# Performance work log

Hardware: AMD Instinct MI355X
Metric: run time of the kernel (lower is better)

Reference implementation:

```python
import jax, jax.numpy as jnp
import numpy as np

B, N, DIM = 16, 1024, 768


def setup_inputs() -> dict:
    key = jax.random.key(0)
    ks = jax.random.split(key, 8)
    x = jax.random.normal(ks[0], (B, N, DIM), dtype=jnp.float32)
    y = jax.random.normal(ks[1], (B, N, DIM), dtype=jnp.float32)
    coords = jax.random.normal(ks[2], (N, N, 6), dtype=jnp.float32)
    # orthogonal init for U (as in torch init.orthogonal_)
    a = jax.random.normal(ks[3], (DIM, DIM), dtype=jnp.float32)
    q, r = jnp.linalg.qr(a)
    U = q * jnp.sign(jnp.diagonal(r))[None, :]
    S1 = jnp.ones((DIM,), dtype=jnp.float32)
    S2 = jnp.ones((DIM,), dtype=jnp.float32)
    gating = jnp.asarray(1.0, dtype=jnp.float32)
    temp = jnp.asarray(0.1, dtype=jnp.float32)
    pos_emb = jnp.zeros((N, 6, 1), dtype=jnp.float32)
    return {"x": x, "y": y, "coords": coords, "U": U, "S1": S1, "S2": S2,
            "gating": gating, "temp": temp, "pos_emb": pos_emb}


def reference(x, y, coords, U, S1, S2, gating, temp, pos_emb):
    dim = x.shape[-1]
    scale = dim ** (-0.5)
    # spectral decomposition: x @ U^T @ diag(S^2) @ U
    xu = x @ U.T                                   # [B,N,d]
    x1 = (xu * jnp.square(S1)) @ U                 # [B,N,d]
    x2 = (xu * jnp.square(S2)) @ U                 # [B,N,d]
    xs = jnp.stack([x1, x2], axis=1)               # [B,2,N,d]
    patch_score = jax.nn.softmax(
        jnp.einsum('bknd,bmd->bknm', xs, y) * scale, axis=-1)  # [B,2,N,M]
    pos = jnp.squeeze(coords @ pos_emb, -1)        # [N,M]
    pos_score = jax.nn.softmax(pos, axis=-1)[None, None]        # [1,1,N,M]
    g = jax.nn.sigmoid(gating)
    attn = (1.0 - g) * patch_score + g * pos_score  # [B,2,N,M]
    # entropy-routed gating
    entropy = jnp.sum(-attn * jnp.log(attn + 1e-8), axis=-1)    # [B,2,N]
    hmap = 2.0 - 2.0 * jax.nn.sigmoid(temp * jnp.transpose(entropy, (0, 2, 1)))  # [B,N,2]
    fgbg = hmap[..., 0] >= hmap[..., 1]
    route = jax.lax.stop_gradient(
        jnp.stack([fgbg, ~fgbg], axis=-1).astype(hmap.dtype))   # [B,N,2]
    heat_map = jnp.sum(hmap * route, axis=-1, keepdims=True)    # [B,N,1]
    attn_c = jnp.sum(attn * jnp.transpose(route, (0, 2, 1))[..., None], axis=1)  # [B,N,M]
    out = attn_c @ y                               # [B,N,d]
    return (out, heat_map)
```

## Files before the change

### kernel.cpp

```cpp
#include <hip/hip_runtime.h>
#include <hip/hip_bf16.h>

#define DEV __device__ __forceinline__

typedef unsigned short u16;
typedef short short8 __attribute__((ext_vector_type(8)));
typedef float f32x16 __attribute__((ext_vector_type(16)));

static const int BB = 16;
static const int NN = 1024;
static const int DD = 768;

DEV u16 f2bf(float f) {
    unsigned u = __builtin_bit_cast(unsigned, f);
    unsigned r = u + 0x7fffu + ((u >> 16) & 1u);
    return (u16)(r >> 16);
}
DEV float h2f(u16 u) { return (float)__builtin_bit_cast(_Float16, u); }
DEV u16 f2h(float f) { return __builtin_bit_cast(u16, (_Float16)f); }

DEV short8 ldf8_bf(const float* p) {
    float4 f0 = *(const float4*)p;
    float4 f1 = *(const float4*)(p + 4);
    short8 r;
    r[0] = (short)f2bf(f0.x); r[1] = (short)f2bf(f0.y);
    r[2] = (short)f2bf(f0.z); r[3] = (short)f2bf(f0.w);
    r[4] = (short)f2bf(f1.x); r[5] = (short)f2bf(f1.y);
    r[6] = (short)f2bf(f1.z); r[7] = (short)f2bf(f1.w);
    return r;
}

DEV void gl_lds16(const u16* g, u16* l) {
    __builtin_amdgcn_global_load_lds(
        (const __attribute__((address_space(1))) unsigned int*)g,
        (__attribute__((address_space(3))) unsigned int*)l, 16, 0, 0);
}

template<int OM>
__global__ __launch_bounds__(256, 3) void gemm128(
    const u16* __restrict__ Ag, const u16* __restrict__ Bg, void* __restrict__ Cg,
    int K, int N, int zmod,
    long sA0, long sA1, long sB0, long sB1, long sC0, long sC1,
    float scale)
{
    __shared__ u16 As[128 * 64];
    __shared__ u16 Bs[128 * 64];

    int z = blockIdx.z;
    const u16* A = Ag + (long)(z % zmod) * sA0 + (long)(z / zmod) * sA1;
    const u16* B = Bg + (long)(z % zmod) * sB0 + (long)(z / zmod) * sB1;
    u16*   Cu = (u16*)Cg   + (long)(z % zmod) * sC0 + (long)(z / zmod) * sC1;
    float* Cf = (float*)Cg + (long)(z % zmod) * sC0 + (long)(z / zmod) * sC1;

    int tid  = threadIdx.x;
    int lane = tid & 63, wave = tid >> 6;
    int wm = wave & 1, wn = wave >> 1;
    int ln31 = lane & 31, khalf = lane >> 5;

    long m0 = (long)blockIdx.x * 128;
    long n0 = (long)blockIdx.y * 128;

    long aOfs[4], bOfs[4];
    u16 *lA[4], *lB[4];
#pragma unroll
    for (int i = 0; i < 4; i++) {
        int p = tid + i * 256;
        int row = p >> 3, qs = p & 7;
        int q = qs ^ (row & 7);
        aOfs[i] = (m0 + row) * (long)K + q * 8;
        bOfs[i] = (n0 + row) * (long)K + q * 8;
        lA[i] = As + p * 8;
        lB[i] = Bs + p * 8;
    }

    int aoff[2][4], boff[2][4];
#pragma unroll
    for (int t = 0; t < 2; t++) {
        int ra = wm * 64 + t * 32 + ln31;
        int rb = wn * 64 + t * 32 + ln31;
#pragma unroll
        for (int h = 0; h < 4; h++) {
            aoff[t][h] = ra * 64 + (((h * 2 + khalf) ^ (ra & 7)) * 8);
            boff[t][h] = rb * 64 + (((h * 2 + khalf) ^ (rb & 7)) * 8);
        }
    }

    f32x16 acc[2][2] = {};

    for (int k0 = 0; k0 < K; k0 += 64) {
#pragma unroll
        for (int i = 0; i < 4; i++) gl_lds16(A + aOfs[i] + k0, lA[i]);
#pragma unroll
        for (int i = 0; i < 4; i++) gl_lds16(B + bOfs[i] + k0, lB[i]);
        __syncthreads();

#pragma unroll
        for (int h = 0; h < 4; h++) {
            short8 af[2], bfr[2];
#pragma unroll
            for (int t = 0; t < 2; t++) af[t]  = *(const short8*)(As + aoff[t][h]);
#pragma unroll
            for (int t = 0; t < 2; t++) bfr[t] = *(const short8*)(Bs + boff[t][h]);
#pragma unroll
            for (int ti = 0; ti < 2; ti++)
#pragma unroll
                for (int tj = 0; tj < 2; tj++)
                    acc[ti][tj] = __builtin_amdgcn_mfma_f32_32x32x16_bf16(
                        af[ti], bfr[tj], acc[ti][tj], 0, 0, 0);
        }
        __syncthreads();
    }

    long crow = m0 + wm * 64 + 4 * khalf;
    long ccol = n0 + wn * 64 + ln31;
#pragma unroll
    for (int ti = 0; ti < 2; ti++)
#pragma unroll
        for (int tj = 0; tj < 2; tj++)
#pragma unroll
            for (int r = 0; r < 16; r++) {
                long row = crow + ti * 32 + (r & 3) + 8 * (r >> 2);
                long col = ccol + tj * 32;
                float v = acc[ti][tj][r] * scale;
                long idx = row * (long)N + col;
                if constexpr (OM == 0)      Cu[idx] = f2bf(v);
                else if constexpr (OM == 1) Cu[idx] = f2h(v);
                else                        Cf[idx] = v;
            }
}

DEV float wave_red_max(float v) {
#pragma unroll
    for (int o = 32; o; o >>= 1) v = fmaxf(v, __shfl_xor(v, o));
    return v;
}
DEV float wave_red_sum(float v) {
#pragma unroll
    for (int o = 32; o; o >>= 1) v += __shfl_xor(v, o);
    return v;
}
DEV float block_red_max(float v, float* sh) {
    v = wave_red_max(v);
    if ((threadIdx.x & 63) == 0) sh[threadIdx.x >> 6] = v;
    __syncthreads();
    v = fmaxf(fmaxf(sh[0], sh[1]), fmaxf(sh[2], sh[3]));
    __syncthreads();
    return v;
}
DEV float block_red_sum(float v, float* sh) {
    v = wave_red_sum(v);
    if ((threadIdx.x & 63) == 0) sh[threadIdx.x >> 6] = v;
    __syncthreads();
    v = (sh[0] + sh[1]) + (sh[2] + sh[3]);
    __syncthreads();
    return v;
}

__global__ __launch_bounds__(256) void k_prep_all(
    const float* __restrict__ x, const float* __restrict__ y,
    const float* __restrict__ coords, const float* __restrict__ U,
    const float* __restrict__ S1, const float* __restrict__ S2,
    const float* __restrict__ pe,
    u16* __restrict__ xb, u16* __restrict__ yb, u16* __restrict__ yT,
    u16* __restrict__ UTb, u16* __restrict__ VT1, u16* __restrict__ VT2,
    float* __restrict__ P)
{
    __shared__ float shmem[32 * 33];
    int bid = blockIdx.x, tid = threadIdx.x;

    if (bid < 6144) {
        long i = ((long)bid * 256 + tid) * 8;
        *(short8*)(xb + i) = ldf8_bf(x + i);
        return;
    }
    bid -= 6144;

    if (bid < 12288) {
        float (*tile)[33] = (float(*)[33])shmem;
        int b = bid / 768, rem = bid % 768;
        int d0 = (rem % 24) * 32, m0 = (rem / 24) * 32;
        int tx = tid & 31, ty = tid >> 5;
        const float* ybase = y + (long)b * NN * DD;
#pragma unroll
        for (int r = 0; r < 32; r += 8) {
            int m = m0 + ty + r, d = d0 + tx;
            float v = ybase[(long)m * DD + d];
            tile[ty + r][tx] = v;
            yb[(long)b * NN * DD + (long)m * DD + d] = f2bf(v);
        }
        __syncthreads();
#pragma unroll
        for (int r = 0; r < 32; r += 8) {
            int d = d0 + ty + r, m = m0 + tx;
            yT[(long)b * DD * NN + (long)d * NN + m] = f2bf(tile[tx][ty + r]);
        }
        return;
    }
    bid -= 12288;

    if (bid < 1024) {
        int n = bid, t = tid;
        float p6[6];
#pragma unroll
        for (int c = 0; c < 6; c++) p6[c] = pe[n * 6 + c];
        float v[4];
#pragma unroll
        for (int i = 0; i < 4; i++) {
            const float* cp = coords + ((long)n * NN + t * 4 + i) * 6;
            v[i] = p6[0]*cp[0] + p6[1]*cp[1] + p6[2]*cp[2]
                 + p6[3]*cp[3] + p6[4]*cp[4] + p6[5]*cp[5];
        }
        float mx = block_red_max(fmaxf(fmaxf(v[0], v[1]), fmaxf(v[2], v[3])), shmem);
        float e[4], s = 0.f;
#pragma unroll
        for (int i = 0; i < 4; i++) { e[i] = expf(v[i] - mx); s += e[i]; }
        float Z = block_red_sum(s, shmem);
        float inv = 1.f / Z;
        float4 o; o.x = e[0]*inv; o.y = e[1]*inv; o.z = e[2]*inv; o.w = e[3]*inv;
        *(float4*)(P + ((long)n << 10) + t * 4) = o;
        return;
    }
    bid -= 1024;

    {
        float (*tile)[33] = (float(*)[33])shmem;
        int i0 = (bid % 24) * 32, j0 = (bid / 24) * 32;
        int tx = tid & 31, ty = tid >> 5;
#pragma unroll
        for (int r = 0; r < 32; r += 8) {
            int i = i0 + ty + r, j = j0 + tx;
            tile[ty + r][tx] = U[(long)i * DD + j];
        }
        __syncthreads();
        float s1v = S1[i0 + tx];
        float s2v = S2[i0 + tx];
        s1v *= s1v; s2v *= s2v;
#pragma unroll
        for (int r = 0; r < 32; r += 8) {
            int j = j0 + ty + r, i = i0 + tx;
            float v = tile[tx][ty + r];
            UTb[(long)j * DD + i] = f2bf(v);
            VT1[(long)j * DD + i] = f2bf(s1v * v);
            VT2[(long)j * DD + i] = f2bf(s2v * v);
        }
    }
}

__global__ __launch_bounds__(256) void k_route(
    u16* __restrict__ S, const float* __restrict__ P,
    const float* __restrict__ gating, const float* __restrict__ temp,
    float* __restrict__ heat)
{
    __shared__ float sh[4];
    int bn = blockIdx.x;
    int b = bn >> 10, n = bn & 1023, t = threadIdx.x;
    u16* s1p = S + ((long)(b * 2) << 20) + ((long)n << 10) + t * 4;
    u16* s2p = s1p + (1L << 20);
    const float* pp = P + ((long)n << 10) + t * 4;

    ushort4 r1 = *(const ushort4*)s1p;
    ushort4 r2 = *(const ushort4*)s2p;
    float4 pv = *(const float4*)pp;
    float s1[4] = { h2f(r1.x), h2f(r1.y), h2f(r1.z), h2f(r1.w) };
    float s2[4] = { h2f(r2.x), h2f(r2.y), h2f(r2.z), h2f(r2.w) };
    float p4[4] = { pv.x, pv.y, pv.z, pv.w };

    float mx1 = block_red_max(fmaxf(fmaxf(s1[0], s1[1]), fmaxf(s1[2], s1[3])), sh);
    float mx2 = block_red_max(fmaxf(fmaxf(s2[0], s2[1]), fmaxf(s2[2], s2[3])), sh);

    float e1[4], e2[4], z1 = 0.f, z2 = 0.f;
#pragma unroll
    for (int i = 0; i < 4; i++) {
        e1[i] = expf(s1[i] - mx1); z1 += e1[i];
        e2[i] = expf(s2[i] - mx2); z2 += e2[i];
    }
    float Z1 = block_red_sum(z1, sh);
    float Z2 = block_red_sum(z2, sh);

    float g = 1.f / (1.f + expf(-gating[0]));
    float c1 = (1.f - g) / Z1, c2 = (1.f - g) / Z2;

    float a1[4], a2[4], hh1 = 0.f, hh2 = 0.f;
#pragma unroll
    for (int i = 0; i < 4; i++) {
        a1[i] = e1[i] * c1 + g * p4[i];
        a2[i] = e2[i] * c2 + g * p4[i];
        hh1 -= a1[i] * logf(a1[i] + 1e-8f);
        hh2 -= a2[i] * logf(a2[i] + 1e-8f);
    }
    float H1 = block_red_sum(hh1, sh);
    float H2 = block_red_sum(hh2, sh);

    float tv = temp[0];
    float hm0 = 2.f - 2.f / (1.f + expf(-tv * H1));
    float hm1 = 2.f - 2.f / (1.f + expf(-tv * H2));
    int ks = (hm0 >= hm1) ? 0 : 1;
    if (t == 0) heat[bn] = ks ? hm1 : hm0;

    ushort4 w;
    w.x = f2bf(ks ? a2[0] : a1[0]);
    w.y = f2bf(ks ? a2[1] : a1[1]);
    w.z = f2bf(ks ? a2[2] : a1[2]);
    w.w = f2bf(ks ? a2[3] : a1[3]);
    *(ushort4*)s1p = w;
}

extern "C" void kernel_launch(void* const* d_in, const int* in_sizes, int n_in,
                              void* d_out, int out_size, void* d_ws, size_t ws_size,
                              hipStream_t stream)
{
    (void)in_sizes; (void)n_in; (void)out_size; (void)ws_size;
    const float* x      = (const float*)d_in[0];
    const float* y      = (const float*)d_in[1];
    const float* coords = (const float*)d_in[2];
    const float* U      = (const float*)d_in[3];
    const float* S1     = (const float*)d_in[4];
    const float* S2     = (const float*)d_in[5];
    const float* gating = (const float*)d_in[6];
    const float* temp   = (const float*)d_in[7];
    const float* pose   = (const float*)d_in[8];

    float* out  = (float*)d_out;
    float* heat = out + (long)BB * NN * DD;

    char* w = (char*)d_ws;
    u16* UTb = (u16*)w;  w += (long)DD * DD * 2;
    u16* VT  = (u16*)w;  w += (long)2 * DD * DD * 2;
    u16* W2  = (u16*)w;  w += (long)2 * DD * DD * 2;
    u16* xb  = (u16*)w;  w += (long)BB * NN * DD * 2;
    u16* x12 = (u16*)w;  w += (long)2 * BB * NN * DD * 2;
    u16* yb  = (u16*)w;  w += (long)BB * NN * DD * 2;
    u16* yT  = (u16*)w;  w += (long)BB * DD * NN * 2;
    u16* S   = (u16*)w;  w += (long)BB * 2 * NN * NN * 2;
    float* P = (float*)w;

    const long MBN = (long)BB * NN * DD;
    const long BND = (long)NN * DD;
    const long SPL = (long)NN * NN;
    const long DSQ = (long)DD * DD;

    k_prep_all<<<dim3(20032), dim3(256), 0, stream>>>(
        x, y, coords, U, S1, S2, pose, xb, yb, yT, UTb, VT, VT + DSQ, P);

    gemm128<0><<<dim3(DD / 128, DD / 128, 2), dim3(256), 0, stream>>>(
        UTb, VT, W2, DD, DD, 2,
        0L, 0L, DSQ, 0L, DSQ, 0L, 1.0f);

    gemm128<0><<<dim3(BB * NN / 128, DD / 128, 2), dim3(256), 0, stream>>>(
        xb, W2, x12, DD, DD, 2,
        0L, 0L, DSQ, 0L, MBN, 0L, 1.0f);

    gemm128<1><<<dim3(NN / 128, NN / 128, BB * 2), dim3(256), 0, stream>>>(
        x12, yb, S, DD, NN, 2,
        MBN, BND, 0L, BND, SPL, 2 * SPL, 0.036084391824351615f);

    k_route<<<dim3(BB * NN), dim3(256), 0, stream>>>(S, P, gating, temp, heat);

    gemm128<2><<<dim3(NN / 128, DD / 128, BB), dim3(256), 0, stream>>>(
        S, yT, out, NN, DD, 1,
        0L, 2 * SPL, 0L, BND, 0L, BND, 1.0f);
}
```

Measured before the change: 384.6 us.

## Fuse x fp32-to-bf16 conversion into GEMM loads and widen route kernel rows

Removes the separate pass that converts x to bf16. A new GEMM variant loads fp32 A tiles straight into LDS and packs them to bf16 with truncating byte permutes before each MFMA. This avoids writing and rereading a bf16 copy of x, at the cost of twice the LDS and global traffic for A tiles and round-toward-zero rather than round-to-nearest conversion. Separately, the routing kernel now uses 128 threads with 8 elements each, so its block reductions span two waves instead of four.

```diff
diff --git a/kernel.cpp b/kernel.cpp
--- a/kernel.cpp
+++ b/kernel.cpp
@@ -30,10 +30,15 @@
     return r;
 }
 
-DEV void gl_lds16(const u16* g, u16* l) {
+DEV void gl_lds16(const void* g, void* l) {
     __builtin_amdgcn_global_load_lds(
         (const __attribute__((address_space(1))) unsigned int*)g,
         (__attribute__((address_space(3))) unsigned int*)l, 16, 0, 0);
+}
+
+DEV unsigned pkbf_rtz(float f0, float f1) {
+    return __builtin_amdgcn_perm(__builtin_bit_cast(unsigned, f1),
+                                 __builtin_bit_cast(unsigned, f0), 0x07060302u);
 }
 
 template<int OM>
@@ -129,6 +134,105 @@
             }
 }
 
+__global__ __launch_bounds__(256, 3) void gemm_f32a(
+    const float* __restrict__ Ag, const u16* __restrict__ Bg, u16* __restrict__ Cg,
+    int K, int N, long sB0, long sC0)
+{
+    __shared__ float As[128 * 64];
+    __shared__ u16   Bs[128 * 64];
+
+    int z = blockIdx.z;
+    const u16* B = Bg + (long)z * sB0;
+    u16* Cu = Cg + (long)z * sC0;
+
+    int tid  = threadIdx.x;
+    int lane = tid & 63, wave = tid >> 6;
+    int wm = wave & 1, wn = wave >> 1;
+    int ln31 = lane & 31, khalf = lane >> 5;
+
+    long m0 = (long)blockIdx.x * 128;
+    long n0 = (long)blockIdx.y * 128;
+
+    long aOfs[8]; float* lA[8];
+#pragma unroll
+    for (int i = 0; i < 8; i++) {
+        int p = tid + i * 256;
+        int row = p >> 4, q = (p & 15) ^ (row & 15);
+        aOfs[i] = (m0 + row) * (long)K + q * 4;
+        lA[i] = As + p * 4;
+    }
+    long bOfs[4]; u16* lB[4];
+#pragma unroll
+    for (int i = 0; i < 4; i++) {
+        int p = tid + i * 256;
+        int row = p >> 3, q = (p & 7) ^ (row & 7);
+        bOfs[i] = (n0 + row) * (long)K + q * 8;
+        lB[i] = Bs + p * 8;
+    }
+
+    int aoff[2][4][2], boff[2][4];
+#pragma unroll
+    for (int t = 0; t < 2; t++) {
+        int ra = wm * 64 + t * 32 + ln31;
+        int rb = wn * 64 + t * 32 + ln31;
+#pragma unroll
+        for (int h = 0; h < 4; h++) {
+            int c0 = h * 4 + khalf * 2;
+            aoff[t][h][0] = ra * 64 + ((c0 ^ (ra & 15)) * 4);
+            aoff[t][h][1] = ra * 64 + (((c0 + 1) ^ (ra & 15)) * 4);
+            boff[t][h] = rb * 64 + (((h * 2 + khalf) ^ (rb & 7)) * 8);
+        }
+    }
+
+    f32x16 acc[2][2] = {};
+
+    for (int k0 = 0; k0 < K; k0 += 64) {
+#pragma unroll
+        for (int i = 0; i < 8; i++) gl_lds16(Ag + aOfs[i] + k0, lA[i]);
+#pragma unroll
+        for (int i = 0; i < 4; i++) gl_lds16(B + bOfs[i] + k0, lB[i]);
+        __syncthreads();
+
+#pragma unroll
+        for (int h = 0; h < 4; h++) {
+            short8 af[2], bfr[2];
+#pragma unroll
+            for (int t = 0; t < 2; t++) {
+                float4 v0 = *(const float4*)(As + aoff[t][h][0]);
+                float4 v1 = *(const float4*)(As + aoff[t][h][1]);
+                uint4 wv;
+                wv.x = pkbf_rtz(v0.x, v0.y);
+                wv.y = pkbf_rtz(v0.z, v0.w);
+                wv.z = pkbf_rtz(v1.x, v1.y);
+                wv.w = pkbf_rtz(v1.z, v1.w);
+                af[t] = __builtin_bit_cast(short8, wv);
+            }
+#pragma unroll
+            for (int t = 0; t < 2; t++) bfr[t] = *(const short8*)(Bs + boff[t][h]);
+#pragma unroll
+            for (int ti = 0; ti < 2; ti++)
+#pragma unroll
+                for (int tj = 0; tj < 2; tj++)
+                    acc[ti][tj] = __builtin_amdgcn_mfma_f32_32x32x16_bf16(
+                        af[ti], bfr[tj], acc[ti][tj], 0, 0, 0);
+        }
+        __syncthreads();
+    }
+
+    long crow = m0 + wm * 64 + 4 * khalf;
+    long ccol = n0 + wn * 64 + ln31;
+#pragma unroll
+    for (int ti = 0; ti < 2; ti++)
+#pragma unroll
+        for (int tj = 0; tj < 2; tj++)
+#pragma unroll
+            for (int r = 0; r < 16; r++) {
+                long row = crow + ti * 32 + (r & 3) + 8 * (r >> 2);
+                long col = ccol + tj * 32;
+                Cu[row * (long)N + col] = f2bf(acc[ti][tj][r]);
+            }
+}
+
 DEV float wave_red_max(float v) {
 #pragma unroll
     for (int o = 32; o; o >>= 1) v = fmaxf(v, __shfl_xor(v, o));
@@ -155,25 +259,34 @@
     __syncthreads();
     return v;
 }
+DEV float red2_max(float v, float* sh) {
+    v = wave_red_max(v);
+    if ((threadIdx.x & 63) == 0) sh[threadIdx.x >> 6] = v;
+    __syncthreads();
+    v = fmaxf(sh[0], sh[1]);
+    __syncthreads();
+    return v;
+}
+DEV float red2_sum(float v, float* sh) {
+    v = wave_red_sum(v);
+    if ((threadIdx.x & 63) == 0) sh[threadIdx.x >> 6] = v;
+    __syncthreads();
+    v = sh[0] + sh[1];
+    __syncthreads();
+    return v;
+}
 
 __global__ __launch_bounds__(256) void k_prep_all(
-    const float* __restrict__ x, const float* __restrict__ y,
+    const float* __restrict__ y,
     const float* __restrict__ coords, const float* __restrict__ U,
     const float* __restrict__ S1, const float* __restrict__ S2,
     const float* __restrict__ pe,
-    u16* __restrict__ xb, u16* __restrict__ yb, u16* __restrict__ yT,
+    u16* __restrict__ yb, u16* __restrict__ yT,
     u16* __restrict__ UTb, u16* __restrict__ VT1, u16* __restrict__ VT2,
     float* __restrict__ P)
 {
     __shared__ float shmem[32 * 33];
     int bid = blockIdx.x, tid = threadIdx.x;
-
-    if (bid < 6144) {
-        long i = ((long)bid * 256 + tid) * 8;
-        *(short8*)(xb + i) = ldf8_bf(x + i);
-        return;
-    }
-    bid -= 6144;
 
     if (bid < 12288) {
         float (*tile)[33] = (float(*)[33])shmem;
@@ -246,50 +359,59 @@
     }
 }
 
-__global__ __launch_bounds__(256) void k_route(
+__global__ __launch_bounds__(128) void k_route(
     u16* __restrict__ S, const float* __restrict__ P,
     const float* __restrict__ gating, const float* __restrict__ temp,
     float* __restrict__ heat)
 {
-    __shared__ float sh[4];
+    __shared__ float sh[2];
     int bn = blockIdx.x;
     int b = bn >> 10, n = bn & 1023, t = threadIdx.x;
-    u16* s1p = S + ((long)(b * 2) << 20) + ((long)n << 10) + t * 4;
+    u16* s1p = S + ((long)(b * 2) << 20) + ((long)n << 10) + t * 8;
     u16* s2p = s1p + (1L << 20);
-    const float* pp = P + ((long)n << 10) + t * 4;
-
-    ushort4 r1 = *(const ushort4*)s1p;
-    ushort4 r2 = *(const ushort4*)s2p;
-    float4 pv = *(const float4*)pp;
-    float s1[4] = { h2f(r1.x), h2f(r1.y), h2f(r1.z), h2f(r1.w) };
-    float s2[4] = { h2f(r2.x), h2f(r2.y), h2f(r2.z), h2f(r2.w) };
-    float p4[4] = { pv.x, pv.y, pv.z, pv.w };
-
-    float mx1 = block_red_max(fmaxf(fmaxf(s1[0], s1[1]), fmaxf(s1[2], s1[3])), sh);
-    float mx2 = block_red_max(fmaxf(fmaxf(s2[0], s2[1]), fmaxf(s2[2], s2[3])), sh);
-
-    float e1[4], e2[4], z1 = 0.f, z2 = 0.f;
-#pragma unroll
-    for (int i = 0; i < 4; i++) {
+    const float* pp = P + ((long)n << 10) + t * 8;
+
+    short8 r1 = *(const short8*)s1p;
+    short8 r2 = *(const short8*)s2p;
+    float4 pv0 = *(const float4*)pp;
+    float4 pv1 = *(const float4*)(pp + 4);
+    float s1[8], s2[8], p8[8];
+#pragma unroll
+    for (int i = 0; i < 8; i++) {
+        s1[i] = h2f((u16)r1[i]);
+        s2[i] = h2f((u16)r2[i]);
+    }
+    p8[0]=pv0.x; p8[1]=pv0.y; p8[2]=pv0.z; p8[3]=pv0.w;
+    p8[4]=pv1.x; p8[5]=pv1.y; p8[6]=pv1.z; p8[7]=pv1.w;
+
+    float m1 = s1[0], m2 = s2[0];
+#pragma unroll
+    for (int i = 1; i < 8; i++) { m1 = fmaxf(m1, s1[i]); m2 = fmaxf(m2, s2[i]); }
+    float mx1 = red2_max(m1, sh);
+    float mx2 = red2_max(m2, sh);
+
+    float e1[8], e2[8], z1 = 0.f, z2 = 0.f;
+#pragma unroll
+    for (int i = 0; i < 8; i++) {
         e1[i] = expf(s1[i] - mx1); z1 += e1[i];
         e2[i] = expf(s2[i] - mx2); z2 += e2[i];
     }
-    float Z1 = block_red_sum(z1, sh);
-    float Z2 = block_red_sum(z2, sh);
+    float Z1 = red2_sum(z1, sh);
+    float Z2 = red2_sum(z2, sh);
 
     float g = 1.f / (1.f + expf(-gating[0]));
     float c1 = (1.f - g) / Z1, c2 = (1.f - g) / Z2;
 
-    float a1[4], a2[4], hh1 = 0.f, hh2 = 0.f;
-#pragma unroll
-    for (int i = 0; i < 4; i++) {
-        a1[i] = e1[i] * c1 + g * p4[i];
-        a2[i] = e2[i] * c2 + g * p4[i];
+    float a1[8], a2[8], hh1 = 0.f, hh2 = 0.f;
+#pragma unroll
+    for (int i = 0; i < 8; i++) {
+        a1[i] = e1[i] * c1 + g * p8[i];
+        a2[i] = e2[i] * c2 + g * p8[i];
         hh1 -= a1[i] * logf(a1[i] + 1e-8f);
         hh2 -= a2[i] * logf(a2[i] + 1e-8f);
     }
-    float H1 = block_red_sum(hh1, sh);
-    float H2 = block_red_sum(hh2, sh);
+    float H1 = red2_sum(hh1, sh);
+    float H2 = red2_sum(hh2, sh);
 
     float tv = temp[0];
     float hm0 = 2.f - 2.f / (1.f + expf(-tv * H1));
@@ -297,12 +419,10 @@
     int ks = (hm0 >= hm1) ? 0 : 1;
     if (t == 0) heat[bn] = ks ? hm1 : hm0;
 
-    ushort4 w;
-    w.x = f2bf(ks ? a2[0] : a1[0]);
-    w.y = f2bf(ks ? a2[1] : a1[1]);
-    w.z = f2bf(ks ? a2[2] : a1[2]);
-    w.w = f2bf(ks ? a2[3] : a1[3]);
-    *(ushort4*)s1p = w;
+    short8 w;
+#pragma unroll
+    for (int i = 0; i < 8; i++) w[i] = (short)f2bf(ks ? a2[i] : a1[i]);
+    *(short8*)s1p = w;
 }
 
 extern "C" void kernel_launch(void* const* d_in, const int* in_sizes, int n_in,
@@ -327,7 +447,6 @@
     u16* UTb = (u16*)w;  w += (long)DD * DD * 2;
     u16* VT  = (u16*)w;  w += (long)2 * DD * DD * 2;
     u16* W2  = (u16*)w;  w += (long)2 * DD * DD * 2;
-    u16* xb  = (u16*)w;  w += (long)BB * NN * DD * 2;
     u16* x12 = (u16*)w;  w += (long)2 * BB * NN * DD * 2;
     u16* yb  = (u16*)w;  w += (long)BB * NN * DD * 2;
     u16* yT  = (u16*)w;  w += (long)BB * DD * NN * 2;
@@ -339,22 +458,21 @@
     const long SPL = (long)NN * NN;
     const long DSQ = (long)DD * DD;
 
-    k_prep_all<<<dim3(20032), dim3(256), 0, stream>>>(
-        x, y, coords, U, S1, S2, pose, xb, yb, yT, UTb, VT, VT + DSQ, P);
+    k_prep_all<<<dim3(13888), dim3(256), 0, stream>>>(
+        y, coords, U, S1, S2, pose, yb, yT, UTb, VT, VT + DSQ, P);
 
     gemm128<0><<<dim3(DD / 128, DD / 128, 2), dim3(256), 0, stream>>>(
         UTb, VT, W2, DD, DD, 2,
         0L, 0L, DSQ, 0L, DSQ, 0L, 1.0f);
 
-    gemm128<0><<<dim3(BB * NN / 128, DD / 128, 2), dim3(256), 0, stream>>>(
-        xb, W2, x12, DD, DD, 2,
-        0L, 0L, DSQ, 0L, MBN, 0L, 1.0f);
+    gemm_f32a<<<dim3(BB * NN / 128, DD / 128, 2), dim3(256), 0, stream>>>(
+        x, W2, x12, DD, DD, DSQ, MBN);
 
     gemm128<1><<<dim3(NN / 128, NN / 128, BB * 2), dim3(256), 0, stream>>>(
         x12, yb, S, DD, NN, 2,
         MBN, BND, 0L, BND, SPL, 2 * SPL, 0.036084391824351615f);
 
-    k_route<<<dim3(BB * NN), dim3(256), 0, stream>>>(S, P, gating, temp, heat);
+    k_route<<<dim3(BB * NN), dim3(128), 0, stream>>>(S, P, gating, temp, heat);
 
     gemm128<2><<<dim3(NN / 128, DD / 128, BB), dim3(256), 0, stream>>>(
         S, yT, out, NN, DD, 1,
```

Measured after the change: 370.2 us. 1.04x faster.
